# Kernel optimization log

Measured on AMD Instinct MI355X. Metric: run time of the kernel, lower is better.

The kernel has to match this reference:

```python
import jax, jax.numpy as jnp
import numpy as np

N_ENT = 50000; N_REL = 200; D = 128; HEADS = 2; ATT_D = 64
E_FULL = 300000; E_BATCH = 80000; NEG_SLOPE = 0.2


def _leaky(x, ns):
    return jnp.where(x >= 0, x, ns * x)


def _gat_conv(x, src, dst, ea, W, We, att_s, att_d, att_e, bias, neg_slope=0.2):
    """PyG GATConv with edge features, add_self_loops=True (fill_value='mean')."""
    N = x.shape[0]
    H, C = att_s.shape
    E = src.shape[0]
    # self-loop edge_attr = mean of incoming edge_attrs per node (PyG fill_value='mean')
    deg = jax.ops.segment_sum(jnp.ones((E,), x.dtype), dst, num_segments=N)
    ea_loop = jax.ops.segment_sum(ea, dst, num_segments=N) / jnp.maximum(deg, 1.0)[:, None]
    loops = jnp.arange(N, dtype=src.dtype)
    src2 = jnp.concatenate([src, loops])
    dst2 = jnp.concatenate([dst, loops])
    ea2 = jnp.concatenate([ea, ea_loop], axis=0)            # [E+N, edge_dim]
    xt = (x @ W).reshape(N, H, C)                            # [N,H,C]
    et = (ea2 @ We).reshape(-1, H, C)                        # [E+N,H,C]
    a_src = jnp.einsum('nhc,hc->nh', xt, att_s)
    a_dst = jnp.einsum('nhc,hc->nh', xt, att_d)
    a_edge = jnp.einsum('ehc,hc->eh', et, att_e)
    alpha = a_src[src2] + a_dst[dst2] + a_edge               # [E+N,H]
    alpha = _leaky(alpha, neg_slope)
    # segment softmax over edges sharing the same target node
    amax = jax.ops.segment_max(alpha, dst2, num_segments=N)
    ex = jnp.exp(alpha - amax[dst2])
    den = jax.ops.segment_sum(ex, dst2, num_segments=N)
    alpha = ex / (den[dst2] + 1e-16)
    out = jax.ops.segment_sum(xt[src2] * alpha[:, :, None], dst2, num_segments=N)
    return out.reshape(N, H * C) + bias


def setup_inputs() -> dict:
    key = jax.random.key(0)
    ks = list(jax.random.split(key, 24))
    p = lambda k, s: jax.random.normal(k, s, dtype=jnp.float32) * 0.05
    s = jax.random.randint(ks[0], (E_FULL,), 0, N_ENT, dtype=jnp.int32)
    r = jax.random.randint(ks[1], (E_FULL,), 0, N_REL, dtype=jnp.int32)
    t = jax.random.randint(ks[2], (E_FULL,), 0, N_ENT, dtype=jnp.int32)
    edge_data = jnp.stack([s, r, t], axis=0)
    edge_index = jax.random.randint(ks[3], (2, E_BATCH), 0, N_ENT, dtype=jnp.int32)
    rel_ids = jax.random.randint(ks[4], (E_BATCH,), 0, N_REL, dtype=jnp.int32)
    edge_attr = jax.nn.one_hot(rel_ids, N_REL, dtype=jnp.float32)
    H1 = HEADS * ATT_D
    H2 = HEADS * D
    return {
        'edge_index': edge_index, 'edge_attr': edge_attr, 'edge_data': edge_data,
        'ent_emb': p(ks[5], (N_ENT, D)), 'rel_emb': p(ks[6], (N_REL, D)),
        'W1': p(ks[7], (D, H1)), 'We1': p(ks[8], (D, H1)),
        'att_s1': p(ks[9], (HEADS, ATT_D)), 'att_d1': p(ks[10], (HEADS, ATT_D)),
        'att_e1': p(ks[11], (HEADS, ATT_D)), 'b1': jnp.zeros((H1,), jnp.float32),
        'W2': p(ks[12], (H1, H2)), 'We2': p(ks[13], (D, H2)),
        'att_s2': p(ks[14], (HEADS, D)), 'att_d2': p(ks[15], (HEADS, D)),
        'att_e2': p(ks[16], (HEADS, D)), 'b2': jnp.zeros((H2,), jnp.float32),
        'W_skip': p(ks[17], (D, D)), 'W_r': p(ks[18], (D, N_REL)),
    }


def reference(edge_index, edge_attr, edge_data, ent_emb, rel_emb, W1, We1, att_s1, att_d1, att_e1, b1, W2, We2, att_s2, att_d2, att_e2, b2, W_skip, W_r):
    src, rel, dst = edge_data[0], edge_data[1], edge_data[2]
    ea = rel_emb[rel]                                        # [E_FULL, D]
    x = _gat_conv(ent_emb, src, dst, ea, W1, We1, att_s1, att_d1, att_e1, b1)
    x = _leaky(x, NEG_SLOPE)                                 # inter-layer act
    x = _gat_conv(x, src, dst, ea, W2, We2, att_s2, att_d2, att_e2, b2)
    # mean over head chunks: [N, H*D] -> [N, D]
    x = x.reshape(N_ENT, HEADS, D).mean(axis=1)
    x = x + ent_emb @ W_skip.T                               # skip connection
    x = x / jnp.maximum(jnp.linalg.norm(x, axis=1, keepdims=True), 1e-12)
    edge_emb = jnp.stack([x[edge_index[0]], x[edge_index[1]]], axis=0)  # [2,EB,D]
    edge_attr_out = edge_attr @ W_r.T                        # [EB, D]
    return edge_emb, edge_attr_out
```

## Files before the change

### kernel.cpp

```cpp
#include <hip/hip_runtime.h>

#define NE 50000
#define NR 200
#define DD 128
#define EF 300000
#define EB 80000
#define NEG 0.2f

typedef unsigned short u16;
typedef u16 u16x8 __attribute__((ext_vector_type(8)));
typedef __bf16 bf16x8 __attribute__((ext_vector_type(8)));
typedef float f32x4 __attribute__((ext_vector_type(4)));

__device__ __forceinline__ float lrelu(float x){ return x >= 0.f ? x : NEG*x; }
__device__ __forceinline__ u16 f2bf(float f){
  unsigned u = __float_as_uint(f);
  u = (u + 0x7FFFu + ((u >> 16) & 1u)) >> 16;
  return (u16)u;
}
__device__ __forceinline__ float bf2f(u16 u){ return __uint_as_float(((unsigned)u) << 16); }

__global__ void k_count(const int* __restrict__ edge_data, int* __restrict__ cnt){
  int e = blockIdx.x*blockDim.x + threadIdx.x;
  if(e < EF) atomicAdd(&cnt[edge_data[2*EF + e]], 1);
}

__global__ void k_scan(const int* __restrict__ cnt, int* __restrict__ row_start){
  __shared__ int wsum[16];
  __shared__ int s_run;
  int tid = threadIdx.x;
  int lane = tid & 63, wv = tid >> 6;
  if(tid==0) s_run = 0;
  __syncthreads();
  const int CH = 4096;
  const int nch = (NE + CH - 1)/CH;
  for(int c=0;c<nch;c++){
    int base = c*CH + tid*4;
    int v0 = base   < NE ? cnt[base]   : 0;
    int v1 = base+1 < NE ? cnt[base+1] : 0;
    int v2 = base+2 < NE ? cnt[base+2] : 0;
    int v3 = base+3 < NE ? cnt[base+3] : 0;
    int tsum = v0+v1+v2+v3;
    int x = tsum;
    #pragma unroll
    for(int o=1;o<64;o<<=1){
      int y = __shfl_up(x, o);
      if(lane >= o) x += y;
    }
    if(lane==63) wsum[wv] = x;
    __syncthreads();
    if(wv==0 && lane<16){
      int w = wsum[lane];
      #pragma unroll
      for(int o=1;o<16;o<<=1){
        int y = __shfl_up(w, o);
        if(lane>=o) w += y;
      }
      wsum[lane] = w;
    }
    __syncthreads();
    int woff = (wv>0) ? wsum[wv-1] : 0;
    int excl = s_run + woff + x - tsum;
    if(base   < NE) row_start[base]   = excl;
    if(base+1 < NE) row_start[base+1] = excl + v0;
    if(base+2 < NE) row_start[base+2] = excl + v0+v1;
    if(base+3 < NE) row_start[base+3] = excl + v0+v1+v2;
    __syncthreads();
    if(tid==1023) s_run += wsum[15];
    __syncthreads();
  }
  if(tid==0) row_start[NE] = s_run;
}

__global__ void k_fill(const int* __restrict__ edge_data, const int* __restrict__ row_start,
                       int* __restrict__ cnt, int* __restrict__ src_s, int* __restrict__ rel_s){
  int e = blockIdx.x*blockDim.x + threadIdx.x;
  if(e < EF){
    int s = edge_data[e], r = edge_data[EF+e], d = edge_data[2*EF+e];
    int pos = row_start[d] + atomicAdd(&cnt[d], 1);
    src_s[pos] = s; rel_s[pos] = r;
  }
}

__global__ void k_vecE(const float* __restrict__ We1, const float* __restrict__ ae1,
                       const float* __restrict__ We2, const float* __restrict__ ae2,
                       float* __restrict__ vecE1, float* __restrict__ vecE2){
  int t = threadIdx.x;
  int d = t>>1, h = t&1;
  float s1 = 0.f;
  for(int c=0;c<64;c++)  s1 += We1[d*128 + h*64  + c]*ae1[h*64  + c];
  vecE1[d*2+h] = s1;
  float s2 = 0.f;
  for(int c=0;c<128;c++) s2 += We2[d*256 + h*128 + c]*ae2[h*128 + c];
  vecE2[d*2+h] = s2;
}

__global__ void k_aE(const float* __restrict__ rel_emb, const float* __restrict__ vecE1,
                     const float* __restrict__ vecE2, float* __restrict__ aE1, float* __restrict__ aE2){
  int r = blockIdx.x, l = threadIdx.x;
  float re0 = rel_emb[r*128 + l], re1 = rel_emb[r*128 + 64 + l];
  float a10 = re0*vecE1[l*2+0] + re1*vecE1[(64+l)*2+0];
  float a11 = re0*vecE1[l*2+1] + re1*vecE1[(64+l)*2+1];
  float a20 = re0*vecE2[l*2+0] + re1*vecE2[(64+l)*2+0];
  float a21 = re0*vecE2[l*2+1] + re1*vecE2[(64+l)*2+1];
  for(int o=32;o;o>>=1){
    a10 += __shfl_xor(a10,o); a11 += __shfl_xor(a11,o);
    a20 += __shfl_xor(a20,o); a21 += __shfl_xor(a21,o);
  }
  if(l==0){ aE1[r*2]=a10; aE1[r*2+1]=a11; aE2[r*2]=a20; aE2[r*2+1]=a21; }
}

__global__ void k_tr(const float* __restrict__ A, float* __restrict__ At, int R, int C){
  int t = blockIdx.x*blockDim.x + threadIdx.x;
  if(t < R*C){ int r = t / C, c = t % C; At[c*R + r] = A[t]; }
}

__global__ void k_prep(const float* __restrict__ W1, const float* __restrict__ Wsk,
                       const float* __restrict__ W2, u16* __restrict__ WT1s, u16* __restrict__ WT2){
  int r = blockIdx.x, k = threadIdx.x;
  if(r < 128)       WT1s[r*128+k] = f2bf(W1[k*128 + r]);
  else if(r < 256)  WT1s[r*128+k] = f2bf(Wsk[(r-128)*128 + k]);
  else              WT2[(r-256)*128+k] = f2bf(W2[k*256 + (r-256)]);
}

template<bool XBF, bool SPLIT>
__global__ __launch_bounds__(256) void k_mgemm(const void* __restrict__ Xv,
    const u16* __restrict__ WT, float* __restrict__ Y0, u16* __restrict__ Yb, int Nrows){
  __shared__ u16 As[64*128];
  __shared__ u16 Bs[64*128];
  int n0 = blockIdx.x*64;
  int cb = blockIdx.y*64;
  int t  = threadIdx.x;
  #pragma unroll
  for(int i=0;i<4;i++){
    int c = i*256 + t;
    int row = c >> 4, kc = c & 15;
    u16x8 pk;
    if(XBF){
      const u16* Xb = (const u16*)Xv;
      if(n0+row < Nrows) pk = *reinterpret_cast<const u16x8*>(&Xb[(size_t)(n0+row)*128 + kc*8]);
      else               pk = (u16x8)(u16)0;
    } else {
      const float* Xf = (const float*)Xv;
      float4 v0 = make_float4(0,0,0,0), v1 = v0;
      if(n0+row < Nrows){
        const float4* p = reinterpret_cast<const float4*>(&Xf[(size_t)(n0+row)*128 + kc*8]);
        v0 = p[0]; v1 = p[1];
      }
      pk[0]=f2bf(v0.x); pk[1]=f2bf(v0.y); pk[2]=f2bf(v0.z); pk[3]=f2bf(v0.w);
      pk[4]=f2bf(v1.x); pk[5]=f2bf(v1.y); pk[6]=f2bf(v1.z); pk[7]=f2bf(v1.w);
    }
    *reinterpret_cast<u16x8*>(&As[row*128 + ((kc ^ (row&7))<<3)]) = pk;
  }
  #pragma unroll
  for(int i=0;i<4;i++){
    int c = i*256 + t;
    int row = c >> 4, kc = c & 15;
    u16x8 pk = *reinterpret_cast<const u16x8*>(&WT[(size_t)(cb+row)*128 + kc*8]);
    *reinterpret_cast<u16x8*>(&Bs[row*128 + ((kc ^ (row&7))<<3)]) = pk;
  }
  __syncthreads();
  int l = t & 63, w = t >> 6;
  int wr = w >> 1, wc = w & 1;
  int lr = l & 15, kg = l >> 4;
  f32x4 acc[2][2] = {};
  const bf16x8* asp = reinterpret_cast<const bf16x8*>(As);
  const bf16x8* bsp = reinterpret_cast<const bf16x8*>(Bs);
  #pragma unroll
  for(int kk=0; kk<4; kk++){
    bf16x8 a[2], b[2];
    #pragma unroll
    for(int m=0;m<2;m++){
      int fr = wr*32 + m*16 + lr;
      a[m] = asp[fr*16 + ((kk*4 + kg) ^ (fr&7))];
    }
    #pragma unroll
    for(int n=0;n<2;n++){
      int fc = wc*32 + n*16 + lr;
      b[n] = bsp[fc*16 + ((kk*4 + kg) ^ (fc&7))];
    }
    #pragma unroll
    for(int m=0;m<2;m++)
      #pragma unroll
      for(int n=0;n<2;n++)
        acc[m][n] = __builtin_amdgcn_mfma_f32_16x16x32_bf16(a[m], b[n], acc[m][n], 0, 0, 0);
  }
  #pragma unroll
  for(int m=0;m<2;m++){
    #pragma unroll
    for(int r=0;r<4;r++){
      int grow = n0 + wr*32 + m*16 + kg*4 + r;
      if(grow >= Nrows) continue;
      #pragma unroll
      for(int n=0;n<2;n++){
        int gcol = cb + wc*32 + n*16 + lr;
        float v = acc[m][n][r];
        if(SPLIT){
          if(cb >= 128) Yb[(size_t)grow*128 + (gcol-128)] = f2bf(v);
          else          Y0[(size_t)grow*128 + gcol] = v;
        } else {
          Y0[(size_t)grow*256 + gcol] = v;
        }
      }
    }
  }
}

template<int C>
__global__ void k_attn(const float* __restrict__ xt, const float* __restrict__ att_s,
                       const float* __restrict__ att_d, float* __restrict__ asrc,
                       float* __restrict__ adst){
  int wv = threadIdx.x>>6, l = threadIdx.x&63;
  int n = blockIdx.x*4 + wv;
  if(n >= NE) return;
  const float* row = xt + (size_t)n*2*C;
  float s0,s1,d0,d1;
  if(C==64){
    float v0=row[l], v1=row[64+l];
    s0 = v0*att_s[l];    s1 = v1*att_s[64+l];
    d0 = v0*att_d[l];    d1 = v1*att_d[64+l];
  } else {
    float v0=row[l], v1=row[64+l], v2=row[128+l], v3=row[192+l];
    s0 = v0*att_s[l] + v1*att_s[64+l];
    s1 = v2*att_s[128+l] + v3*att_s[192+l];
    d0 = v0*att_d[l] + v1*att_d[64+l];
    d1 = v2*att_d[128+l] + v3*att_d[192+l];
  }
  for(int o=32;o;o>>=1){
    s0+=__shfl_xor(s0,o); s1+=__shfl_xor(s1,o);
    d0+=__shfl_xor(d0,o); d1+=__shfl_xor(d1,o);
  }
  if(l==0){ asrc[n*2]=s0; asrc[n*2+1]=s1; adst[n*2]=d0; adst[n*2+1]=d1; }
}

template<int C, bool LK, bool OUTBF>
__global__ __launch_bounds__(256) void k_agg(const float* __restrict__ xt,
    const float* __restrict__ asrc, const float* __restrict__ adst,
    const float* __restrict__ aE, const int* __restrict__ row_start,
    const int* __restrict__ src_s, const int* __restrict__ rel_s,
    const float* __restrict__ bias, void* __restrict__ outv){
  constexpr int HC = 2*C;
  constexpr int NJ = HC/64;
  int wv = threadIdx.x>>6, l = threadIdx.x&63;
  int n = blockIdx.x*4 + wv;
  if(n >= NE) return;
  int b = row_start[n], e = row_start[n+1];
  int deg = e - b;
  float2 ad = *reinterpret_cast<const float2*>(&adst[n*2]);
  float sE0=0.f, sE1=0.f;
  for(int i=b;i<e;i++){
    float2 a = *reinterpret_cast<const float2*>(&aE[rel_s[i]*2]);
    sE0 += a.x; sE1 += a.y;
  }
  float invdeg = 1.f/fmaxf((float)deg, 1.f);
  float2 asn = *reinterpret_cast<const float2*>(&asrc[n*2]);
  float m0 = lrelu(asn.x + ad.x + sE0*invdeg);
  float m1 = lrelu(asn.y + ad.y + sE1*invdeg);
  float den0=1.f, den1=1.f;
  float acc[NJ];
  #pragma unroll
  for(int j=0;j<NJ;j++) acc[j] = xt[(size_t)n*HC + j*64 + l];
  for(int i=b;i<e;i++){
    int s = src_s[i], r = rel_s[i];
    float2 as = *reinterpret_cast<const float2*>(&asrc[s*2]);
    float2 ae = *reinterpret_cast<const float2*>(&aE[r*2]);
    float l0 = lrelu(as.x + ad.x + ae.x);
    float l1 = lrelu(as.y + ad.y + ae.y);
    float nm0 = fmaxf(m0,l0), nm1 = fmaxf(m1,l1);
    float sc0 = __expf(m0-nm0), sc1 = __expf(m1-nm1);
    float w0  = __expf(l0-nm0), w1  = __expf(l1-nm1);
    den0 = den0*sc0 + w0; den1 = den1*sc1 + w1;
    m0 = nm0; m1 = nm1;
    #pragma unroll
    for(int j=0;j<NJ;j++){
      float sc = ((j*64)/C == 0) ? sc0 : sc1;
      float w  = ((j*64)/C == 0) ? w0  : w1;
      acc[j] = acc[j]*sc + w * xt[(size_t)s*HC + j*64 + l];
    }
  }
  float i0 = 1.f/(den0 + 1e-16f), i1 = 1.f/(den1 + 1e-16f);
  #pragma unroll
  for(int j=0;j<NJ;j++){
    int comp = j*64 + l;
    float v = acc[j] * (((j*64)/C == 0) ? i0 : i1) + bias[comp];
    if(LK) v = lrelu(v);
    if(OUTBF) ((u16*)outv)[(size_t)n*HC + comp] = f2bf(v);
    else      ((float*)outv)[(size_t)n*HC + comp] = v;
  }
}

__global__ void k_combine(const float* __restrict__ out2, const u16* __restrict__ skip,
                          float* __restrict__ xf){
  int wv = threadIdx.x>>6, l = threadIdx.x&63;
  int n = blockIdx.x*4 + wv;
  if(n >= NE) return;
  float v0 = 0.5f*(out2[(size_t)n*256 + l]      + out2[(size_t)n*256 + 128 + l]) + bf2f(skip[(size_t)n*128 + l]);
  float v1 = 0.5f*(out2[(size_t)n*256 + 64 + l] + out2[(size_t)n*256 + 192 + l]) + bf2f(skip[(size_t)n*128 + 64 + l]);
  float ss = v0*v0 + v1*v1;
  for(int o=32;o;o>>=1) ss += __shfl_xor(ss,o);
  float inv = 1.f/fmaxf(sqrtf(ss), 1e-12f);
  xf[(size_t)n*128 + l]      = v0*inv;
  xf[(size_t)n*128 + 64 + l] = v1*inv;
}

__global__ void k_gather(const int* __restrict__ ei, const float* __restrict__ xf,
                         float* __restrict__ out){
  int wv = threadIdx.x>>6, l = threadIdx.x&63;
  int e = blockIdx.x*4 + wv;
  if(e >= EB) return;
  int i0 = ei[e], i1 = ei[EB + e];
  out[(size_t)e*128 + l]                     = xf[(size_t)i0*128 + l];
  out[(size_t)e*128 + 64 + l]                = xf[(size_t)i0*128 + 64 + l];
  out[(size_t)EB*128 + (size_t)e*128 + l]    = xf[(size_t)i1*128 + l];
  out[(size_t)EB*128 + (size_t)e*128 + 64+l] = xf[(size_t)i1*128 + 64 + l];
}

__global__ void k_attr(const float* __restrict__ ea, const float* __restrict__ Wrt,
                       float* __restrict__ out){
  int wv = threadIdx.x>>6, l = threadIdx.x&63;
  int e = blockIdx.x*4 + wv;
  if(e >= EB) return;
  const float* row = ea + (size_t)e*NR;
  float acc0=0.f, acc1=0.f;
  #pragma unroll
  for(int ch=0; ch<4; ch++){
    int idx = ch*64 + l;
    float v = (idx < NR) ? row[idx] : 0.f;
    unsigned long long mask = __ballot(v != 0.f);
    while(mask){
      int bit = __builtin_ctzll(mask);
      mask &= mask - 1;
      int r = ch*64 + bit;
      float vv = __shfl(v, bit);
      acc0 += vv * Wrt[r*128 + l];
      acc1 += vv * Wrt[r*128 + 64 + l];
    }
  }
  out[(size_t)e*128 + l]      = acc0;
  out[(size_t)e*128 + 64 + l] = acc1;
}

extern "C" void kernel_launch(void* const* d_in, const int* in_sizes, int n_in,
                              void* d_out, int out_size, void* d_ws, size_t ws_size,
                              hipStream_t stream){
  const int*   edge_index = (const int*)  d_in[0];
  const float* edge_attr  = (const float*)d_in[1];
  const int*   edge_data  = (const int*)  d_in[2];
  const float* ent_emb    = (const float*)d_in[3];
  const float* rel_emb    = (const float*)d_in[4];
  const float* W1     = (const float*)d_in[5];
  const float* We1    = (const float*)d_in[6];
  const float* att_s1 = (const float*)d_in[7];
  const float* att_d1 = (const float*)d_in[8];
  const float* att_e1 = (const float*)d_in[9];
  const float* b1     = (const float*)d_in[10];
  const float* W2     = (const float*)d_in[11];
  const float* We2    = (const float*)d_in[12];
  const float* att_s2 = (const float*)d_in[13];
  const float* att_d2 = (const float*)d_in[14];
  const float* att_e2 = (const float*)d_in[15];
  const float* b2     = (const float*)d_in[16];
  const float* W_skip = (const float*)d_in[17];
  const float* W_r    = (const float*)d_in[18];
  float* out = (float*)d_out;

  char* ws = (char*)d_ws;
  size_t off = 0;
  auto alloc = [&](size_t bytes){ void* p = ws + off; off += (bytes + 255) & ~(size_t)255; return p; };
  int*   cnt       = (int*)  alloc((size_t)NE*4);
  int*   row_start = (int*)  alloc((size_t)(NE+1)*4);
  int*   src_s     = (int*)  alloc((size_t)EF*4);
  int*   rel_s     = (int*)  alloc((size_t)EF*4);
  float* vecE1     = (float*)alloc(128*2*4);
  float* vecE2     = (float*)alloc(128*2*4);
  float* aE1       = (float*)alloc(NR*2*4);
  float* aE2       = (float*)alloc(NR*2*4);
  float* asrc1     = (float*)alloc((size_t)NE*2*4);
  float* adst1     = (float*)alloc((size_t)NE*2*4);
  float* asrc2     = (float*)alloc((size_t)NE*2*4);
  float* adst2     = (float*)alloc((size_t)NE*2*4);
  u16*   WT1s      = (u16*)  alloc(256*128*2);
  u16*   WT2      = (u16*)  alloc(256*128*2);
  float* Wrt       = (float*)alloc(NR*128*4);
  float* xt1       = (float*)alloc((size_t)NE*128*4);
  u16*   skip      = (u16*)  alloc((size_t)NE*128*2);
  u16*   h1        = (u16*)  alloc((size_t)NE*128*2);
  float* xf = xt1;
  float* xt2  = out;
  float* out2 = out + (size_t)NE*256;

  hipMemsetAsync(cnt, 0, (size_t)NE*4, stream);
  k_count<<<(EF+255)/256, 256, 0, stream>>>(edge_data, cnt);
  k_scan<<<1, 1024, 0, stream>>>(cnt, row_start);
  hipMemsetAsync(cnt, 0, (size_t)NE*4, stream);
  k_fill<<<(EF+255)/256, 256, 0, stream>>>(edge_data, row_start, cnt, src_s, rel_s);
  k_vecE<<<1, 256, 0, stream>>>(We1, att_e1, We2, att_e2, vecE1, vecE2);
  k_aE<<<NR, 64, 0, stream>>>(rel_emb, vecE1, vecE2, aE1, aE2);
  k_prep<<<512, 128, 0, stream>>>(W1, W_skip, W2, WT1s, WT2);

  dim3 gg((NE+63)/64, 4);
  k_mgemm<false, true><<<gg, 256, 0, stream>>>(ent_emb, WT1s, xt1, skip, NE);
  k_attn<64><<<(NE+3)/4, 256, 0, stream>>>(xt1, att_s1, att_d1, asrc1, adst1);
  k_agg<64, true, true><<<(NE+3)/4, 256, 0, stream>>>(xt1, asrc1, adst1, aE1, row_start, src_s, rel_s, b1, h1);

  k_mgemm<true, false><<<gg, 256, 0, stream>>>(h1, WT2, xt2, nullptr, NE);
  k_attn<128><<<(NE+3)/4, 256, 0, stream>>>(xt2, att_s2, att_d2, asrc2, adst2);
  k_agg<128, false, false><<<(NE+3)/4, 256, 0, stream>>>(xt2, asrc2, adst2, aE2, row_start, src_s, rel_s, b2, out2);

  k_combine<<<(NE+3)/4, 256, 0, stream>>>(out2, skip, xf);

  k_tr<<<(128*NR+255)/256, 256, 0, stream>>>(W_r, Wrt, 128, NR);
  k_gather<<<(EB+3)/4, 256, 0, stream>>>(edge_index, xf, out);
  k_attr<<<(EB+3)/4, 256, 0, stream>>>(edge_attr, Wrt, out + (size_t)2*EB*128);
}
```

Baseline: 575.0 us.

## Store GAT intermediates in bf16 and loop column blocks inside GEMM

The projected node features xt1/xt2 and the normalized final embeddings are now stored as bf16 instead of fp32, and the attention, aggregation, combine and gather kernels read them as packed pairs. This roughly halves the bytes moved by the gather-heavy aggregation. The GEMM now loops over the four column blocks inside one workgroup, so the A tile is loaded once instead of once per column block. Aggregation caches the edge-attention table in shared memory and folds the self-loop mean into the main edge loop rather than making a separate pass. The trade-off is extra rounding, which adds precision risk in the aggregated features and the final outputs.

```diff
diff --git a/kernel.cpp b/kernel.cpp
--- a/kernel.cpp
+++ b/kernel.cpp
@@ -2,12 +2,13 @@
 
 #define NE 50000
 #define NR 200
-#define DD 128
 #define EF 300000
 #define EB 80000
 #define NEG 0.2f
+#define NINF (-1e30f)
 
 typedef unsigned short u16;
+typedef unsigned int u32;
 typedef u16 u16x8 __attribute__((ext_vector_type(8)));
 typedef __bf16 bf16x8 __attribute__((ext_vector_type(8)));
 typedef float f32x4 __attribute__((ext_vector_type(4)));
@@ -19,6 +20,8 @@
   return (u16)u;
 }
 __device__ __forceinline__ float bf2f(u16 u){ return __uint_as_float(((unsigned)u) << 16); }
+__device__ __forceinline__ float bflo(u32 p){ return __uint_as_float(p << 16); }
+__device__ __forceinline__ float bfhi(u32 p){ return __uint_as_float(p & 0xFFFF0000u); }
 
 __global__ void k_count(const int* __restrict__ edge_data, int* __restrict__ cnt){
   int e = blockIdx.x*blockDim.x + threadIdx.x;
@@ -125,11 +128,10 @@
 
 template<bool XBF, bool SPLIT>
 __global__ __launch_bounds__(256) void k_mgemm(const void* __restrict__ Xv,
-    const u16* __restrict__ WT, float* __restrict__ Y0, u16* __restrict__ Yb, int Nrows){
+    const u16* __restrict__ WT, u16* __restrict__ Y0, u16* __restrict__ Yb, int Nrows){
   __shared__ u16 As[64*128];
   __shared__ u16 Bs[64*128];
   int n0 = blockIdx.x*64;
-  int cb = blockIdx.y*64;
   int t  = threadIdx.x;
   #pragma unroll
   for(int i=0;i<4;i++){
@@ -152,118 +154,126 @@
     }
     *reinterpret_cast<u16x8*>(&As[row*128 + ((kc ^ (row&7))<<3)]) = pk;
   }
-  #pragma unroll
-  for(int i=0;i<4;i++){
-    int c = i*256 + t;
-    int row = c >> 4, kc = c & 15;
-    u16x8 pk = *reinterpret_cast<const u16x8*>(&WT[(size_t)(cb+row)*128 + kc*8]);
-    *reinterpret_cast<u16x8*>(&Bs[row*128 + ((kc ^ (row&7))<<3)]) = pk;
-  }
-  __syncthreads();
   int l = t & 63, w = t >> 6;
   int wr = w >> 1, wc = w & 1;
   int lr = l & 15, kg = l >> 4;
-  f32x4 acc[2][2] = {};
   const bf16x8* asp = reinterpret_cast<const bf16x8*>(As);
   const bf16x8* bsp = reinterpret_cast<const bf16x8*>(Bs);
-  #pragma unroll
-  for(int kk=0; kk<4; kk++){
-    bf16x8 a[2], b[2];
-    #pragma unroll
-    for(int m=0;m<2;m++){
-      int fr = wr*32 + m*16 + lr;
-      a[m] = asp[fr*16 + ((kk*4 + kg) ^ (fr&7))];
-    }
-    #pragma unroll
-    for(int n=0;n<2;n++){
-      int fc = wc*32 + n*16 + lr;
-      b[n] = bsp[fc*16 + ((kk*4 + kg) ^ (fc&7))];
-    }
-    #pragma unroll
-    for(int m=0;m<2;m++)
+  for(int cbi=0; cbi<4; cbi++){
+    int cb = cbi*64;
+    #pragma unroll
+    for(int i=0;i<4;i++){
+      int c = i*256 + t;
+      int row = c >> 4, kc = c & 15;
+      u16x8 pk = *reinterpret_cast<const u16x8*>(&WT[(size_t)(cb+row)*128 + kc*8]);
+      *reinterpret_cast<u16x8*>(&Bs[row*128 + ((kc ^ (row&7))<<3)]) = pk;
+    }
+    __syncthreads();
+    f32x4 acc[2][2] = {};
+    #pragma unroll
+    for(int kk=0; kk<4; kk++){
+      bf16x8 a[2], b[2];
       #pragma unroll
-      for(int n=0;n<2;n++)
-        acc[m][n] = __builtin_amdgcn_mfma_f32_16x16x32_bf16(a[m], b[n], acc[m][n], 0, 0, 0);
-  }
-  #pragma unroll
-  for(int m=0;m<2;m++){
-    #pragma unroll
-    for(int r=0;r<4;r++){
-      int grow = n0 + wr*32 + m*16 + kg*4 + r;
-      if(grow >= Nrows) continue;
+      for(int m=0;m<2;m++){
+        int fr = wr*32 + m*16 + lr;
+        a[m] = asp[fr*16 + ((kk*4 + kg) ^ (fr&7))];
+      }
       #pragma unroll
       for(int n=0;n<2;n++){
-        int gcol = cb + wc*32 + n*16 + lr;
-        float v = acc[m][n][r];
-        if(SPLIT){
-          if(cb >= 128) Yb[(size_t)grow*128 + (gcol-128)] = f2bf(v);
-          else          Y0[(size_t)grow*128 + gcol] = v;
-        } else {
-          Y0[(size_t)grow*256 + gcol] = v;
+        int fc = wc*32 + n*16 + lr;
+        b[n] = bsp[fc*16 + ((kk*4 + kg) ^ (fc&7))];
+      }
+      #pragma unroll
+      for(int m=0;m<2;m++)
+        #pragma unroll
+        for(int n=0;n<2;n++)
+          acc[m][n] = __builtin_amdgcn_mfma_f32_16x16x32_bf16(a[m], b[n], acc[m][n], 0, 0, 0);
+    }
+    #pragma unroll
+    for(int m=0;m<2;m++){
+      #pragma unroll
+      for(int r=0;r<4;r++){
+        int grow = n0 + wr*32 + m*16 + kg*4 + r;
+        if(grow < Nrows){
+          #pragma unroll
+          for(int n=0;n<2;n++){
+            int gcol = cb + wc*32 + n*16 + lr;
+            u16 v = f2bf(acc[m][n][r]);
+            if(SPLIT){
+              if(cb >= 128) Yb[(size_t)grow*128 + (gcol-128)] = v;
+              else          Y0[(size_t)grow*128 + gcol] = v;
+            } else {
+              Y0[(size_t)grow*256 + gcol] = v;
+            }
+          }
         }
       }
     }
+    __syncthreads();
   }
 }
 
 template<int C>
-__global__ void k_attn(const float* __restrict__ xt, const float* __restrict__ att_s,
+__global__ void k_attn(const u16* __restrict__ xt, const float* __restrict__ att_s,
                        const float* __restrict__ att_d, float* __restrict__ asrc,
                        float* __restrict__ adst){
   int wv = threadIdx.x>>6, l = threadIdx.x&63;
   int n = blockIdx.x*4 + wv;
   if(n >= NE) return;
-  const float* row = xt + (size_t)n*2*C;
-  float s0,s1,d0,d1;
+  const u32* row = reinterpret_cast<const u32*>(xt) + (size_t)n*C;
   if(C==64){
-    float v0=row[l], v1=row[64+l];
-    s0 = v0*att_s[l];    s1 = v1*att_s[64+l];
-    d0 = v0*att_d[l];    d1 = v1*att_d[64+l];
+    u32 p = row[l];
+    float x0 = bflo(p), x1 = bfhi(p);
+    float sl = x0*att_s[2*l] + x1*att_s[2*l+1];
+    float dl = x0*att_d[2*l] + x1*att_d[2*l+1];
+    #pragma unroll
+    for(int o=16;o;o>>=1){ sl += __shfl_xor(sl,o); dl += __shfl_xor(dl,o); }
+    if(l==0){  asrc[n*2]   = sl; adst[n*2]   = dl; }
+    if(l==32){ asrc[n*2+1] = sl; adst[n*2+1] = dl; }
   } else {
-    float v0=row[l], v1=row[64+l], v2=row[128+l], v3=row[192+l];
-    s0 = v0*att_s[l] + v1*att_s[64+l];
-    s1 = v2*att_s[128+l] + v3*att_s[192+l];
-    d0 = v0*att_d[l] + v1*att_d[64+l];
-    d1 = v2*att_d[128+l] + v3*att_d[192+l];
-  }
-  for(int o=32;o;o>>=1){
-    s0+=__shfl_xor(s0,o); s1+=__shfl_xor(s1,o);
-    d0+=__shfl_xor(d0,o); d1+=__shfl_xor(d1,o);
-  }
-  if(l==0){ asrc[n*2]=s0; asrc[n*2+1]=s1; adst[n*2]=d0; adst[n*2+1]=d1; }
+    u32 p0 = row[l], p1 = row[64+l];
+    float x00 = bflo(p0), x01 = bfhi(p0), x10 = bflo(p1), x11 = bfhi(p1);
+    float s0 = x00*att_s[2*l]     + x01*att_s[2*l+1];
+    float s1 = x10*att_s[128+2*l] + x11*att_s[128+2*l+1];
+    float d0 = x00*att_d[2*l]     + x01*att_d[2*l+1];
+    float d1 = x10*att_d[128+2*l] + x11*att_d[128+2*l+1];
+    #pragma unroll
+    for(int o=32;o;o>>=1){
+      s0+=__shfl_xor(s0,o); s1+=__shfl_xor(s1,o);
+      d0+=__shfl_xor(d0,o); d1+=__shfl_xor(d1,o);
+    }
+    if(l==0){ asrc[n*2]=s0; asrc[n*2+1]=s1; adst[n*2]=d0; adst[n*2+1]=d1; }
+  }
 }
 
 template<int C, bool LK, bool OUTBF>
-__global__ __launch_bounds__(256) void k_agg(const float* __restrict__ xt,
+__global__ __launch_bounds__(256) void k_agg(const u16* __restrict__ xt,
     const float* __restrict__ asrc, const float* __restrict__ adst,
     const float* __restrict__ aE, const int* __restrict__ row_start,
     const int* __restrict__ src_s, const int* __restrict__ rel_s,
     const float* __restrict__ bias, void* __restrict__ outv){
-  constexpr int HC = 2*C;
-  constexpr int NJ = HC/64;
-  int wv = threadIdx.x>>6, l = threadIdx.x&63;
+  constexpr int NP = C/64;
+  __shared__ float2 sAE[NR];
+  int tid = threadIdx.x;
+  for(int i=tid; i<NR; i+=256) sAE[i] = reinterpret_cast<const float2*>(aE)[i];
+  __syncthreads();
+  int wv = tid>>6, l = tid&63;
   int n = blockIdx.x*4 + wv;
   if(n >= NE) return;
   int b = row_start[n], e = row_start[n+1];
   int deg = e - b;
-  float2 ad = *reinterpret_cast<const float2*>(&adst[n*2]);
-  float sE0=0.f, sE1=0.f;
-  for(int i=b;i<e;i++){
-    float2 a = *reinterpret_cast<const float2*>(&aE[rel_s[i]*2]);
-    sE0 += a.x; sE1 += a.y;
-  }
-  float invdeg = 1.f/fmaxf((float)deg, 1.f);
+  float2 ad  = *reinterpret_cast<const float2*>(&adst[n*2]);
   float2 asn = *reinterpret_cast<const float2*>(&asrc[n*2]);
-  float m0 = lrelu(asn.x + ad.x + sE0*invdeg);
-  float m1 = lrelu(asn.y + ad.y + sE1*invdeg);
-  float den0=1.f, den1=1.f;
-  float acc[NJ];
+  const u32* xtu = reinterpret_cast<const u32*>(xt);
+  float m0=NINF, m1=NINF, den0=0.f, den1=0.f, sE0=0.f, sE1=0.f;
+  float acc[NP][2];
   #pragma unroll
-  for(int j=0;j<NJ;j++) acc[j] = xt[(size_t)n*HC + j*64 + l];
+  for(int j=0;j<NP;j++){ acc[j][0]=0.f; acc[j][1]=0.f; }
   for(int i=b;i<e;i++){
     int s = src_s[i], r = rel_s[i];
     float2 as = *reinterpret_cast<const float2*>(&asrc[s*2]);
-    float2 ae = *reinterpret_cast<const float2*>(&aE[r*2]);
+    float2 ae = sAE[r];
+    sE0 += ae.x; sE1 += ae.y;
     float l0 = lrelu(as.x + ad.x + ae.x);
     float l1 = lrelu(as.y + ad.y + ae.y);
     float nm0 = fmaxf(m0,l0), nm1 = fmaxf(m1,l1);
@@ -272,47 +282,76 @@
     den0 = den0*sc0 + w0; den1 = den1*sc1 + w1;
     m0 = nm0; m1 = nm1;
     #pragma unroll
-    for(int j=0;j<NJ;j++){
-      float sc = ((j*64)/C == 0) ? sc0 : sc1;
-      float w  = ((j*64)/C == 0) ? w0  : w1;
-      acc[j] = acc[j]*sc + w * xt[(size_t)s*HC + j*64 + l];
+    for(int j=0;j<NP;j++){
+      u32 p = xtu[(size_t)s*C + j*64 + l];
+      float sc, w;
+      if(C==64){ sc = (l<32)?sc0:sc1; w = (l<32)?w0:w1; }
+      else     { sc = (j==0)?sc0:sc1; w = (j==0)?w0:w1; }
+      acc[j][0] = acc[j][0]*sc + w*bflo(p);
+      acc[j][1] = acc[j][1]*sc + w*bfhi(p);
+    }
+  }
+  {
+    float invdeg = 1.f/fmaxf((float)deg, 1.f);
+    float l0 = lrelu(asn.x + ad.x + sE0*invdeg);
+    float l1 = lrelu(asn.y + ad.y + sE1*invdeg);
+    float nm0 = fmaxf(m0,l0), nm1 = fmaxf(m1,l1);
+    float sc0 = __expf(m0-nm0), sc1 = __expf(m1-nm1);
+    float w0  = __expf(l0-nm0), w1  = __expf(l1-nm1);
+    den0 = den0*sc0 + w0; den1 = den1*sc1 + w1;
+    #pragma unroll
+    for(int j=0;j<NP;j++){
+      u32 p = xtu[(size_t)n*C + j*64 + l];
+      float sc, w;
+      if(C==64){ sc = (l<32)?sc0:sc1; w = (l<32)?w0:w1; }
+      else     { sc = (j==0)?sc0:sc1; w = (j==0)?w0:w1; }
+      acc[j][0] = acc[j][0]*sc + w*bflo(p);
+      acc[j][1] = acc[j][1]*sc + w*bfhi(p);
     }
   }
   float i0 = 1.f/(den0 + 1e-16f), i1 = 1.f/(den1 + 1e-16f);
   #pragma unroll
-  for(int j=0;j<NJ;j++){
-    int comp = j*64 + l;
-    float v = acc[j] * (((j*64)/C == 0) ? i0 : i1) + bias[comp];
-    if(LK) v = lrelu(v);
-    if(OUTBF) ((u16*)outv)[(size_t)n*HC + comp] = f2bf(v);
-    else      ((float*)outv)[(size_t)n*HC + comp] = v;
+  for(int j=0;j<NP;j++){
+    float ih;
+    if(C==64) ih = (l<32)?i0:i1; else ih = (j==0)?i0:i1;
+    float2 bp = reinterpret_cast<const float2*>(bias)[j*64 + l];
+    float v0 = acc[j][0]*ih + bp.x;
+    float v1 = acc[j][1]*ih + bp.y;
+    if(LK){ v0 = lrelu(v0); v1 = lrelu(v1); }
+    if(OUTBF){
+      ((u32*)outv)[(size_t)n*C + j*64 + l] = (u32)f2bf(v0) | ((u32)f2bf(v1)<<16);
+    } else {
+      reinterpret_cast<float2*>(outv)[(size_t)n*(C) + j*64 + l] = make_float2(v0, v1);
+    }
   }
 }
 
 __global__ void k_combine(const float* __restrict__ out2, const u16* __restrict__ skip,
-                          float* __restrict__ xf){
+                          u16* __restrict__ xf){
   int wv = threadIdx.x>>6, l = threadIdx.x&63;
   int n = blockIdx.x*4 + wv;
   if(n >= NE) return;
-  float v0 = 0.5f*(out2[(size_t)n*256 + l]      + out2[(size_t)n*256 + 128 + l]) + bf2f(skip[(size_t)n*128 + l]);
-  float v1 = 0.5f*(out2[(size_t)n*256 + 64 + l] + out2[(size_t)n*256 + 192 + l]) + bf2f(skip[(size_t)n*128 + 64 + l]);
+  const float2* o2 = reinterpret_cast<const float2*>(out2) + (size_t)n*128;
+  float2 a0 = o2[l], a1 = o2[64+l];
+  u32 sp = reinterpret_cast<const u32*>(skip)[(size_t)n*64 + l];
+  float v0 = 0.5f*(a0.x + a1.x) + bflo(sp);
+  float v1 = 0.5f*(a0.y + a1.y) + bfhi(sp);
   float ss = v0*v0 + v1*v1;
   for(int o=32;o;o>>=1) ss += __shfl_xor(ss,o);
   float inv = 1.f/fmaxf(sqrtf(ss), 1e-12f);
-  xf[(size_t)n*128 + l]      = v0*inv;
-  xf[(size_t)n*128 + 64 + l] = v1*inv;
-}
-
-__global__ void k_gather(const int* __restrict__ ei, const float* __restrict__ xf,
+  reinterpret_cast<u32*>(xf)[(size_t)n*64 + l] = (u32)f2bf(v0*inv) | ((u32)f2bf(v1*inv)<<16);
+}
+
+__global__ void k_gather(const int* __restrict__ ei, const u16* __restrict__ xf,
                          float* __restrict__ out){
   int wv = threadIdx.x>>6, l = threadIdx.x&63;
   int e = blockIdx.x*4 + wv;
   if(e >= EB) return;
   int i0 = ei[e], i1 = ei[EB + e];
-  out[(size_t)e*128 + l]                     = xf[(size_t)i0*128 + l];
-  out[(size_t)e*128 + 64 + l]                = xf[(size_t)i0*128 + 64 + l];
-  out[(size_t)EB*128 + (size_t)e*128 + l]    = xf[(size_t)i1*128 + l];
-  out[(size_t)EB*128 + (size_t)e*128 + 64+l] = xf[(size_t)i1*128 + 64 + l];
+  u32 p0 = reinterpret_cast<const u32*>(xf)[(size_t)i0*64 + l];
+  u32 p1 = reinterpret_cast<const u32*>(xf)[(size_t)i1*64 + l];
+  reinterpret_cast<float2*>(out)[(size_t)e*64 + l] = make_float2(bflo(p0), bfhi(p0));
+  reinterpret_cast<float2*>(out + (size_t)EB*128)[(size_t)e*64 + l] = make_float2(bflo(p1), bfhi(p1));
 }
 
 __global__ void k_attr(const float* __restrict__ ea, const float* __restrict__ Wrt,
@@ -349,12 +388,12 @@
   const float* ent_emb    = (const float*)d_in[3];
   const float* rel_emb    = (const float*)d_in[4];
   const float* W1     = (const float*)d_in[5];
-  const float* We1    = (const float*)d_in[6];
   const float* att_s1 = (const float*)d_in[7];
   const float* att_d1 = (const float*)d_in[8];
   const float* att_e1 = (const float*)d_in[9];
   const float* b1     = (const float*)d_in[10];
   const float* W2     = (const float*)d_in[11];
+  const float* We1    = (const float*)d_in[6];
   const float* We2    = (const float*)d_in[12];
   const float* att_s2 = (const float*)d_in[13];
   const float* att_d2 = (const float*)d_in[14];
@@ -380,14 +419,14 @@
   float* asrc2     = (float*)alloc((size_t)NE*2*4);
   float* adst2     = (float*)alloc((size_t)NE*2*4);
   u16*   WT1s      = (u16*)  alloc(256*128*2);
-  u16*   WT2      = (u16*)  alloc(256*128*2);
+  u16*   WT2       = (u16*)  alloc(256*128*2);
   float* Wrt       = (float*)alloc(NR*128*4);
-  float* xt1       = (float*)alloc((size_t)NE*128*4);
+  u16*   xt1       = (u16*)  alloc((size_t)NE*128*2);
   u16*   skip      = (u16*)  alloc((size_t)NE*128*2);
   u16*   h1        = (u16*)  alloc((size_t)NE*128*2);
-  float* xf = xt1;
-  float* xt2  = out;
-  float* out2 = out + (size_t)NE*256;
+  u16*   xf = xt1;
+  u16*   xt2  = (u16*)out;
+  float* out2 = out + (size_t)NE*128;
 
   hipMemsetAsync(cnt, 0, (size_t)NE*4, stream);
   k_count<<<(EF+255)/256, 256, 0, stream>>>(edge_data, cnt);
@@ -397,8 +436,9 @@
   k_vecE<<<1, 256, 0, stream>>>(We1, att_e1, We2, att_e2, vecE1, vecE2);
   k_aE<<<NR, 64, 0, stream>>>(rel_emb, vecE1, vecE2, aE1, aE2);
   k_prep<<<512, 128, 0, stream>>>(W1, W_skip, W2, WT1s, WT2);
-
-  dim3 gg((NE+63)/64, 4);
+  k_tr<<<(128*NR+255)/256, 256, 0, stream>>>(W_r, Wrt, 128, NR);
+
+  int gg = (NE+63)/64;
   k_mgemm<false, true><<<gg, 256, 0, stream>>>(ent_emb, WT1s, xt1, skip, NE);
   k_attn<64><<<(NE+3)/4, 256, 0, stream>>>(xt1, att_s1, att_d1, asrc1, adst1);
   k_agg<64, true, true><<<(NE+3)/4, 256, 0, stream>>>(xt1, asrc1, adst1, aE1, row_start, src_s, rel_s, b1, h1);
@@ -409,7 +449,6 @@
 
   k_combine<<<(NE+3)/4, 256, 0, stream>>>(out2, skip, xf);
 
-  k_tr<<<(128*NR+255)/256, 256, 0, stream>>>(W_r, Wrt, 128, NR);
   k_gather<<<(EB+3)/4, 256, 0, stream>>>(edge_index, xf, out);
   k_attr<<<(EB+3)/4, 256, 0, stream>>>(edge_attr, Wrt, out + (size_t)2*EB*128);
 }
```

Result: faster. 492.0 us (-14.4%).
